# Optimization experiments

Measured on AMD Instinct MI355X. Metric: run time of the kernel, lower is better.

The kernel has to match this reference:

```python
import jax, jax.numpy as jnp
import numpy as np

B, S, D, H = 2, 2048, 1024, 16
DK = D // H

def setup_inputs() -> dict:
    key = jax.random.key(0)
    ks = jax.random.split(key, 11)
    sc = 1.0 / np.sqrt(D)
    return {
        "q": jax.random.normal(ks[0], (B, S, D), jnp.float32),
        "k": jax.random.normal(ks[1], (B, S, D), jnp.float32),
        "v": jax.random.normal(ks[2], (B, S, D), jnp.float32),
        "Wq": jax.random.normal(ks[3], (D, D), jnp.float32) * sc,
        "bq": jax.random.normal(ks[4], (D,), jnp.float32) * sc,
        "Wk": jax.random.normal(ks[5], (D, D), jnp.float32) * sc,
        "bk": jax.random.normal(ks[6], (D,), jnp.float32) * sc,
        "Wv": jax.random.normal(ks[7], (D, D), jnp.float32) * sc,
        "bv": jax.random.normal(ks[8], (D,), jnp.float32) * sc,
        "Wo": jax.random.normal(ks[9], (D, D), jnp.float32) * sc,
        "bo": jax.random.normal(ks[10], (D,), jnp.float32) * sc,
    }

def reference(q, k, v, Wq, bq, Wk, bk, Wv, bv, Wo, bo):
    b, s, d = q.shape
    # projections (torch Linear: x @ W^T + b)
    qh = (q @ Wq.T + bq).reshape(b, s, H, DK).transpose(0, 2, 1, 3)  # [B,H,S,DK]
    kh = (k @ Wk.T + bk).reshape(b, s, H, DK).transpose(0, 2, 1, 3)
    vh = (v @ Wv.T + bv).reshape(b, s, H, DK).transpose(0, 2, 1, 3)
    scores = jnp.einsum('bhqd,bhkd->bhqk', qh, kh) / jnp.sqrt(jnp.float32(DK))
    attn = jax.nn.softmax(scores, axis=-1)  # [B,H,S,S]
    out = jnp.einsum('bhqk,bhkd->bhqd', attn, vh)  # [B,H,S,DK]
    out = out.transpose(0, 2, 1, 3).reshape(b, s, d)
    return out @ Wo.T + bo
```

## Files before the change

### kernel.cpp

```cpp
#include <hip/hip_runtime.h>
#include <hip/hip_bf16.h>
#include <stdint.h>

typedef __bf16 bf16;
typedef __attribute__((ext_vector_type(8))) __bf16 bf16x8;
typedef __attribute__((ext_vector_type(4))) float f32x4;
typedef __attribute__((ext_vector_type(16))) float f32x16;
typedef __attribute__((ext_vector_type(4))) unsigned int u32x4;
typedef __attribute__((ext_vector_type(2))) unsigned int u32x2;

#define BATCH  2
#define SEQ    2048
#define DMODEL 1024
#define NH     16
#define DKH    64
#define BS     (BATCH*SEQ)
#define BSD    (BS*DMODEL)
#define DD     (DMODEL*DMODEL)

#define QSCALE 0.18033688f

__device__ __forceinline__ void gload_lds16(const bf16* g, bf16* l) {
  __builtin_amdgcn_global_load_lds((const __attribute__((address_space(1))) void*)g,
                                   (__attribute__((address_space(3))) void*)l,
                                   16, 0, 0);
}

__device__ __forceinline__ unsigned int packbf2(float a, float b) {
  union { bf16 h[2]; unsigned int u; } z;
  z.h[0] = (bf16)a; z.h[1] = (bf16)b;
  return z.u;
}

__device__ __forceinline__ float exp2_raw(float x) {
  float r;
  asm("v_exp_f32 %0, %1" : "=v"(r) : "v"(x));
  return r;
}

__device__ __forceinline__ void cvt8(const float* __restrict__ in,
                                     bf16* __restrict__ out, int i) {
  const f32x4* p = (const f32x4*)in + (size_t)i * 2;
  f32x4 a = p[0], b = p[1];
  bf16x8 o;
  o[0]=(bf16)a[0]; o[1]=(bf16)a[1]; o[2]=(bf16)a[2]; o[3]=(bf16)a[3];
  o[4]=(bf16)b[0]; o[5]=(bf16)b[1]; o[6]=(bf16)b[2]; o[7]=(bf16)b[3];
  ((bf16x8*)out)[i] = o;
}

__global__ __launch_bounds__(256) void cvt_all_kernel(
    const float* __restrict__ q, const float* __restrict__ k, const float* __restrict__ v,
    const float* __restrict__ Wq, const float* __restrict__ Wk,
    const float* __restrict__ Wv, const float* __restrict__ Wo,
    bf16* __restrict__ oq, bf16* __restrict__ ok, bf16* __restrict__ ov,
    bf16* __restrict__ oWq, bf16* __restrict__ oWk,
    bf16* __restrict__ oWv, bf16* __restrict__ oWo) {
  int i = blockIdx.x * blockDim.x + threadIdx.x;
  const int z = blockIdx.y;
  if (z == 0)      cvt8(q, oq, i);
  else if (z == 1) cvt8(k, ok, i);
  else if (z == 2) cvt8(v, ov, i);
  else {
    const int w = i >> 17;
    const int j = i & 131071;
    const float* in = (w == 0) ? Wq : (w == 1) ? Wk : (w == 2) ? Wv : Wo;
    bf16* out       = (w == 0) ? oWq : (w == 1) ? oWk : (w == 2) ? oWv : oWo;
    cvt8(in, out, j);
  }
}

template <typename OUT, int MODE, int MR>
__device__ __forceinline__ void gemm_body(const bf16* __restrict__ A,
                                          const bf16* __restrict__ W,
                                          const float* __restrict__ bias,
                                          OUT* __restrict__ C,
                                          float oscale,
                                          bf16* Als, bf16* Bls,
                                          int tx, int ty) {
  const int tid  = threadIdx.x;
  const int lane = tid & 63;
  const int wave = tid >> 6;
  const int wm = wave >> 1, wn = wave & 1;
  const int c = lane & 15, g = lane >> 4;
  const long brow = (long)ty * (MR * 32);
  const long bcol = (long)tx * 128;
  const int  N = DMODEL, K = DMODEL;
  const int  ABUF = MR * 1024;

  f32x4 acc[MR][4] = {};

  const bf16* Ag = A + (brow + wave*16 + ((lane>>2)&15)) * (long)K + (lane & 3) * 8;
  const bf16* Bg = W + (bcol + wave*16 + ((lane>>2)&15)) * (long)K + (lane & 3) * 8;

  auto stage = [&](int kt, int buf) {
    const bf16* a0 = Ag + kt * 32;
    const bf16* b0 = Bg + kt * 32;
    bf16* Ad = Als + buf * ABUF + wave * 512;
    bf16* Bd = Bls + buf * 4096 + wave * 512;
    gload_lds16(a0, Ad);
    if (MR == 4) gload_lds16(a0 + 64 * (long)K, Ad + 2048);
    gload_lds16(b0, Bd);
    gload_lds16(b0 + 64 * (long)K, Bd + 2048);
  };

  const int nk = K >> 5;
  stage(0, 0);
  int cur = 0;
  for (int kt = 0; kt < nk; ++kt) {
    __syncthreads();
    if (kt + 1 < nk) stage(kt + 1, cur ^ 1);

    bf16x8 af[MR], bfv[4];
    #pragma unroll
    for (int m = 0; m < MR; ++m)
      af[m] = *(const bf16x8*)(Als + cur * ABUF + (wm*(MR*16) + m*16 + c) * 32 + g * 8);
    #pragma unroll
    for (int n = 0; n < 4; ++n)
      bfv[n] = *(const bf16x8*)(Bls + cur * 4096 + (wn*64 + n*16 + c) * 32 + g * 8);
    __builtin_amdgcn_s_setprio(1);
    #pragma unroll
    for (int m = 0; m < MR; ++m)
      #pragma unroll
      for (int n = 0; n < 4; ++n)
        acc[m][n] = __builtin_amdgcn_mfma_f32_16x16x32_bf16(af[m], bfv[n], acc[m][n], 0, 0, 0);
    __builtin_amdgcn_s_setprio(0);
    cur ^= 1;
  }

  if (MODE == 0) {
    #pragma unroll
    for (int n = 0; n < 4; ++n) {
      const long col = bcol + wn*64 + n*16 + c;
      const float bb = bias[col];
      #pragma unroll
      for (int m = 0; m < MR; ++m) {
        #pragma unroll
        for (int r = 0; r < 4; ++r) {
          const long row = brow + wm*(MR*16) + m*16 + g*4 + r;
          C[row * (long)N + col] = (OUT)((acc[m][n][r] + bb) * oscale);
        }
      }
    }
  } else {
    const int srow = (int)(brow & (SEQ - 1));
    const int bidx = (int)(brow >> 11);
    #pragma unroll
    for (int n = 0; n < 4; ++n) {
      const int col = (int)bcol + wn*64 + n*16 + c;
      const float bb = bias[col];
      const int h = col >> 6, dk = col & 63;
      OUT* rowp = C + ((size_t)((bidx*16 + h)*64 + dk)) * SEQ + srow + wm*64;
      #pragma unroll
      for (int m = 0; m < MR; ++m) {
        u32x2 pkd;
        pkd[0] = packbf2(acc[m][n][0] + bb, acc[m][n][1] + bb);
        pkd[1] = packbf2(acc[m][n][2] + bb, acc[m][n][3] + bb);
        *(u32x2*)(rowp + m*16 + g*4) = pkd;
      }
    }
  }
}

__global__ __launch_bounds__(256) void gemm_qkv_kernel(
    const bf16* __restrict__ qb, const bf16* __restrict__ kb, const bf16* __restrict__ vb,
    const bf16* __restrict__ Wqb, const bf16* __restrict__ Wkb, const bf16* __restrict__ Wvb,
    const float* __restrict__ bq, const float* __restrict__ bk, const float* __restrict__ bv,
    bf16* __restrict__ qh, bf16* __restrict__ kh, bf16* __restrict__ vt) {
  __shared__ bf16 Als[2 * 128 * 32];
  __shared__ bf16 Bls[2 * 128 * 32];
  const int bid  = blockIdx.x + (blockIdx.y << 3) + (blockIdx.z << 8);
  const int tile = (bid & 7) * 96 + (bid >> 3);
  const int tx = tile & 7, ty = (tile >> 3) & 31, tz = tile >> 8;
  if (tz == 2) {
    gemm_body<bf16, 1, 4>(vb, Wvb, bv, vt, 1.0f, Als, Bls, tx, ty);
  } else {
    const bf16*  A  = (tz == 0) ? qb  : kb;
    const bf16*  W  = (tz == 0) ? Wqb : Wkb;
    const float* bi = (tz == 0) ? bq  : bk;
    bf16*        Cp = (tz == 0) ? qh  : kh;
    const float  os = (tz == 0) ? QSCALE : 1.0f;
    gemm_body<bf16, 0, 4>(A, W, bi, Cp, os, Als, Bls, tx, ty);
  }
}

__global__ __launch_bounds__(256) void gemm_out_kernel(
    const bf16* __restrict__ A, const bf16* __restrict__ Wob,
    const float* __restrict__ bo, float* __restrict__ C) {
  __shared__ bf16 Als[2 * 64 * 32];
  __shared__ bf16 Bls[2 * 128 * 32];
  const int bid  = blockIdx.x + (blockIdx.y << 3);
  const int tile = (bid & 7) * 64 + (bid >> 3);
  const int tx = tile & 7, ty = tile >> 3;
  gemm_body<float, 0, 2>(A, Wob, bo, C, 1.0f, Als, Bls, tx, ty);
}

__global__ __launch_bounds__(256) void attn_kernel(const bf16* __restrict__ qh,
                                                   const bf16* __restrict__ kh,
                                                   const bf16* __restrict__ vt,
                                                   bf16* __restrict__ ao) {
  __shared__ bf16 Kls[2][64 * 64];
  __shared__ bf16 Vls[2][64 * 64];

  const int tid = threadIdx.x;
  const int lane = tid & 63, wave = tid >> 6;
  const int q32 = lane & 31, hi = lane >> 5;

  const int bx  = blockIdx.x;
  const int bh  = (bx & 7) * 4 + ((bx >> 3) >> 4);
  const int qt  = (bx >> 3) & 15;
  const int b = bh >> 4, h = bh & 15;
  const long rowbase = (long)b * SEQ;
  const int q0 = qt * 128 + wave * 32;

  const bf16* qp = qh + (rowbase + q0 + q32) * DMODEL + h * 64 + hi * 8;
  bf16x8 qf[4];
  #pragma unroll
  for (int ks = 0; ks < 4; ++ks) qf[ks] = *(const bf16x8*)(qp + ks * 16);

  f32x16 accO0 = {}, accO1 = {};
  f32x16 accL  = {};

  bf16x8 ones8;
  {
    const bf16 sel = (q32 == 0) ? (bf16)1.0f : (bf16)0.0f;
    #pragma unroll
    for (int j = 0; j < 8; ++j) ones8[j] = sel;
  }

  int rd[2][4];
  #pragma unroll
  for (int hh = 0; hh < 2; ++hh) {
    const int row = q32 + 32 * hh;
    const int sw = (row & 7) << 4;
    #pragma unroll
    for (int ks = 0; ks < 4; ++ks)
      rd[hh][ks] = row * 128 + ((ks * 32 + hi * 16) ^ sw);
  }

  const int srw = tid >> 3, stc = tid & 7;
  const int soff = srw * 128 + ((stc * 16) ^ ((srw & 7) << 4));
  u32x4 kreg0, kreg1, vreg0, vreg1;

  const bf16* kp = kh + (rowbase + srw) * DMODEL + h * 64 + stc * 8;
  const bf16* vp = vt + ((size_t)bh * 64 + srw) * SEQ + stc * 8;

  auto load_tiles = [&]() {
    kreg0 = *(const u32x4*)kp;
    kreg1 = *(const u32x4*)(kp + 32 * DMODEL);
    vreg0 = *(const u32x4*)vp;
    vreg1 = *(const u32x4*)(vp + 32 * SEQ);
    kp += 64 * DMODEL;
    vp += 64;
  };
  auto write_tiles = [&](int buf) {
    char* Kb = (char*)Kls[buf];
    char* Vb = (char*)Vls[buf];
    *(u32x4*)(Kb + soff)        = kreg0;
    *(u32x4*)(Kb + soff + 4096) = kreg1;
    *(u32x4*)(Vb + soff)        = vreg0;
    *(u32x4*)(Vb + soff + 4096) = vreg1;
  };

  load_tiles();
  write_tiles(0);
  int cur = 0;
  const int NT = SEQ / 64;

  for (int t = 0; t < NT; ++t) {
    __syncthreads();
    if (t + 1 < NT) load_tiles();

    const char* Kb = (const char*)Kls[cur];
    const char* Vb = (const char*)Vls[cur];

    f32x16 s0 = {}, s1 = {};
    __builtin_amdgcn_s_setprio(1);
    #pragma unroll
    for (int ks = 0; ks < 4; ++ks) {
      bf16x8 k0 = *(const bf16x8*)(Kb + rd[0][ks]);
      s0 = __builtin_amdgcn_mfma_f32_32x32x16_bf16(k0, qf[ks], s0, 0, 0, 0);
    }
    #pragma unroll
    for (int ks = 0; ks < 4; ++ks) {
      bf16x8 k1 = *(const bf16x8*)(Kb + rd[1][ks]);
      s1 = __builtin_amdgcn_mfma_f32_32x32x16_bf16(k1, qf[ks], s1, 0, 0, 0);
    }
    __builtin_amdgcn_s_setprio(0);

    unsigned W0[4][2], W1[4][2];
    #pragma unroll
    for (int t4 = 0; t4 < 4; ++t4) {
      float a0 = exp2_raw(s0[4*t4+0]), a1 = exp2_raw(s0[4*t4+1]);
      float a2 = exp2_raw(s0[4*t4+2]), a3 = exp2_raw(s0[4*t4+3]);
      W0[t4][0] = packbf2(a0, a1); W0[t4][1] = packbf2(a2, a3);
      float b0 = exp2_raw(s1[4*t4+0]), b1 = exp2_raw(s1[4*t4+1]);
      float b2 = exp2_raw(s1[4*t4+2]), b3 = exp2_raw(s1[4*t4+3]);
      W1[t4][0] = packbf2(b0, b1); W1[t4][1] = packbf2(b2, b3);
    }

    bf16x8 Pb[4];
    #pragma unroll
    for (int ks = 0; ks < 4; ++ks) {
      const int t0 = 2 * (ks & 1);
      unsigned w0 = (ks < 2) ? W0[t0][0]     : W1[t0][0];
      unsigned w2 = (ks < 2) ? W0[t0 + 1][0] : W1[t0 + 1][0];
      unsigned w1 = (ks < 2) ? W0[t0][1]     : W1[t0][1];
      unsigned w3 = (ks < 2) ? W0[t0 + 1][1] : W1[t0 + 1][1];
      asm("v_permlane32_swap_b32 %0, %1" : "+v"(w0), "+v"(w2));
      asm("v_permlane32_swap_b32 %0, %1" : "+v"(w1), "+v"(w3));
      union { unsigned u[4]; bf16x8 v; } P;
      P.u[0] = w0; P.u[1] = w1; P.u[2] = w2; P.u[3] = w3;
      Pb[ks] = P.v;
    }

    __builtin_amdgcn_s_setprio(1);
    #pragma unroll
    for (int ks = 0; ks < 4; ++ks) {
      bf16x8 v0 = *(const bf16x8*)(Vb + rd[0][ks]);
      accO0 = __builtin_amdgcn_mfma_f32_32x32x16_bf16(v0, Pb[ks], accO0, 0, 0, 0);
    }
    #pragma unroll
    for (int ks = 0; ks < 4; ++ks) {
      bf16x8 v1 = *(const bf16x8*)(Vb + rd[1][ks]);
      accO1 = __builtin_amdgcn_mfma_f32_32x32x16_bf16(v1, Pb[ks], accO1, 0, 0, 0);
    }
    #pragma unroll
    for (int ks = 0; ks < 4; ++ks)
      accL = __builtin_amdgcn_mfma_f32_32x32x16_bf16(ones8, Pb[ks], accL, 0, 0, 0);
    __builtin_amdgcn_s_setprio(0);

    if (t + 1 < NT) write_tiles(cur ^ 1);
    cur ^= 1;
  }

  const float lall = __shfl(accL[0], q32);
  const float inv = 1.f / lall;
  bf16* dst = ao + (rowbase + q0 + q32) * DMODEL + h * 64;
  #pragma unroll
  for (int t4 = 0; t4 < 4; ++t4) {
    const int d0 = 8 * t4 + 4 * hi;
    u32x2 p0, p1;
    p0[0] = packbf2(accO0[4*t4+0] * inv, accO0[4*t4+1] * inv);
    p0[1] = packbf2(accO0[4*t4+2] * inv, accO0[4*t4+3] * inv);
    *(u32x2*)(dst + d0) = p0;
    p1[0] = packbf2(accO1[4*t4+0] * inv, accO1[4*t4+1] * inv);
    p1[1] = packbf2(accO1[4*t4+2] * inv, accO1[4*t4+3] * inv);
    *(u32x2*)(dst + d0 + 32) = p1;
  }
}

extern "C" void kernel_launch(void* const* d_in, const int* in_sizes, int n_in,
                              void* d_out, int out_size, void* d_ws, size_t ws_size,
                              hipStream_t stream) {
  const float* q  = (const float*)d_in[0];
  const float* k  = (const float*)d_in[1];
  const float* v  = (const float*)d_in[2];
  const float* Wq = (const float*)d_in[3];
  const float* bq = (const float*)d_in[4];
  const float* Wk = (const float*)d_in[5];
  const float* bk = (const float*)d_in[6];
  const float* Wv = (const float*)d_in[7];
  const float* bv = (const float*)d_in[8];
  const float* Wo = (const float*)d_in[9];
  const float* bo = (const float*)d_in[10];
  float* out = (float*)d_out;

  char* w = (char*)d_ws;
  bf16* qb  = (bf16*)w; w += (size_t)BSD * 2;
  bf16* kb  = (bf16*)w; w += (size_t)BSD * 2;
  bf16* vb  = (bf16*)w; w += (size_t)BSD * 2;
  bf16* Wqb = (bf16*)w; w += (size_t)DD * 2;
  bf16* Wkb = (bf16*)w; w += (size_t)DD * 2;
  bf16* Wvb = (bf16*)w; w += (size_t)DD * 2;
  bf16* Wob = (bf16*)w; w += (size_t)DD * 2;
  bf16* qhd = (bf16*)w; w += (size_t)BSD * 2;
  bf16* khd = (bf16*)w; w += (size_t)BSD * 2;
  bf16* vtd = (bf16*)w; w += (size_t)BSD * 2;
  bf16* aod = (bf16*)w; w += (size_t)BSD * 2;

  cvt_all_kernel<<<dim3(BSD / 8 / 256, 4), 256, 0, stream>>>(
      q, k, v, Wq, Wk, Wv, Wo, qb, kb, vb, Wqb, Wkb, Wvb, Wob);

  gemm_qkv_kernel<<<dim3(8, 32, 3), 256, 0, stream>>>(qb, kb, vb, Wqb, Wkb, Wvb,
                                                      bq, bk, bv, qhd, khd, vtd);
  attn_kernel<<<512, 256, 0, stream>>>(qhd, khd, vtd, aod);
  gemm_out_kernel<<<dim3(8, 64), 256, 0, stream>>>(aod, Wob, bo, out);
}
```

Measured before the change: 128.8 us.

## Split attention KV sequence across two wave groups per block and reduce in LDS

Doubles the attention block to 512 threads: each pair of waves shares a 32-row query slice but processes opposite halves of the key/value sequence, staging both halves' tiles into a 64KB LDS buffer. Partial output and row-sum accumulators are then combined through shared memory before normalization and store. The aim is more waves in flight per CU to hide the serial KV-loop latency, at the cost of higher LDS use, which may limit occupancy, plus an extra reduction step. The softmax has no max subtraction, so the partial sums can be added directly.

```diff
diff --git a/kernel.cpp b/kernel.cpp
--- a/kernel.cpp
+++ b/kernel.cpp
@@ -194,23 +194,25 @@
   gemm_body<float, 0, 2>(A, Wob, bo, C, 1.0f, Als, Bls, tx, ty);
 }
 
-__global__ __launch_bounds__(256) void attn_kernel(const bf16* __restrict__ qh,
+__global__ __launch_bounds__(512) void attn_kernel(const bf16* __restrict__ qh,
                                                    const bf16* __restrict__ kh,
                                                    const bf16* __restrict__ vt,
                                                    bf16* __restrict__ ao) {
-  __shared__ bf16 Kls[2][64 * 64];
-  __shared__ bf16 Vls[2][64 * 64];
+  __shared__ char smem[65536];
+  bf16* Kbase = (bf16*)smem;
+  bf16* Vbase = (bf16*)(smem + 32768);
 
   const int tid = threadIdx.x;
   const int lane = tid & 63, wave = tid >> 6;
   const int q32 = lane & 31, hi = lane >> 5;
+  const int qg = wave >> 1, half = wave & 1;
 
   const int bx  = blockIdx.x;
   const int bh  = (bx & 7) * 4 + ((bx >> 3) >> 4);
   const int qt  = (bx >> 3) & 15;
   const int b = bh >> 4, h = bh & 15;
   const long rowbase = (long)b * SEQ;
-  const int q0 = qt * 128 + wave * 32;
+  const int q0 = qt * 128 + qg * 32;
 
   const bf16* qp = qh + (rowbase + q0 + q32) * DMODEL + h * 64 + hi * 8;
   bf16x8 qf[4];
@@ -237,12 +239,14 @@
       rd[hh][ks] = row * 128 + ((ks * 32 + hi * 16) ^ sw);
   }
 
-  const int srw = tid >> 3, stc = tid & 7;
+  const int st_half = tid >> 8;
+  const int t8 = tid & 255;
+  const int srw = t8 >> 3, stc = t8 & 7;
   const int soff = srw * 128 + ((stc * 16) ^ ((srw & 7) << 4));
   u32x4 kreg0, kreg1, vreg0, vreg1;
 
-  const bf16* kp = kh + (rowbase + srw) * DMODEL + h * 64 + stc * 8;
-  const bf16* vp = vt + ((size_t)bh * 64 + srw) * SEQ + stc * 8;
+  const bf16* kp = kh + (rowbase + st_half * 1024 + srw) * DMODEL + h * 64 + stc * 8;
+  const bf16* vp = vt + ((size_t)bh * 64 + srw) * SEQ + st_half * 1024 + stc * 8;
 
   auto load_tiles = [&]() {
     kreg0 = *(const u32x4*)kp;
@@ -253,8 +257,8 @@
     vp += 64;
   };
   auto write_tiles = [&](int buf) {
-    char* Kb = (char*)Kls[buf];
-    char* Vb = (char*)Vls[buf];
+    char* Kb = (char*)(Kbase + (buf * 2 + st_half) * 4096);
+    char* Vb = (char*)(Vbase + (buf * 2 + st_half) * 4096);
     *(u32x4*)(Kb + soff)        = kreg0;
     *(u32x4*)(Kb + soff + 4096) = kreg1;
     *(u32x4*)(Vb + soff)        = vreg0;
@@ -264,14 +268,14 @@
   load_tiles();
   write_tiles(0);
   int cur = 0;
-  const int NT = SEQ / 64;
-
-  for (int t = 0; t < NT; ++t) {
+  const int NT2 = SEQ / 64 / 2;
+
+  for (int t = 0; t < NT2; ++t) {
     __syncthreads();
-    if (t + 1 < NT) load_tiles();
-
-    const char* Kb = (const char*)Kls[cur];
-    const char* Vb = (const char*)Vls[cur];
+    if (t + 1 < NT2) load_tiles();
+
+    const char* Kb = (const char*)(Kbase + (cur * 2 + half) * 4096);
+    const char* Vb = (const char*)(Vbase + (cur * 2 + half) * 4096);
 
     f32x16 s0 = {}, s1 = {};
     __builtin_amdgcn_s_setprio(1);
@@ -329,23 +333,42 @@
       accL = __builtin_amdgcn_mfma_f32_32x32x16_bf16(ones8, Pb[ks], accL, 0, 0, 0);
     __builtin_amdgcn_s_setprio(0);
 
-    if (t + 1 < NT) write_tiles(cur ^ 1);
+    if (t + 1 < NT2) write_tiles(cur ^ 1);
     cur ^= 1;
   }
 
-  const float lall = __shfl(accL[0], q32);
-  const float inv = 1.f / lall;
-  bf16* dst = ao + (rowbase + q0 + q32) * DMODEL + h * 64;
-  #pragma unroll
-  for (int t4 = 0; t4 < 4; ++t4) {
-    const int d0 = 8 * t4 + 4 * hi;
-    u32x2 p0, p1;
-    p0[0] = packbf2(accO0[4*t4+0] * inv, accO0[4*t4+1] * inv);
-    p0[1] = packbf2(accO0[4*t4+2] * inv, accO0[4*t4+3] * inv);
-    *(u32x2*)(dst + d0) = p0;
-    p1[0] = packbf2(accO1[4*t4+0] * inv, accO1[4*t4+1] * inv);
-    p1[1] = packbf2(accO1[4*t4+2] * inv, accO1[4*t4+3] * inv);
-    *(u32x2*)(dst + d0 + 32) = p1;
+  const float lpart = __shfl(accL[0], q32);
+  __syncthreads();
+  float* cb = (float*)smem + qg * 2176;
+  if (half == 1) {
+    #pragma unroll
+    for (int i = 0; i < 16; ++i) {
+      cb[lane + 64 * i]        = accO0[i];
+      cb[lane + 64 * (16 + i)] = accO1[i];
+    }
+    cb[lane + 64 * 32] = lpart;
+  }
+  __syncthreads();
+  if (half == 0) {
+    const float lall = lpart + cb[lane + 64 * 32];
+    const float inv = 1.f / lall;
+    #pragma unroll
+    for (int i = 0; i < 16; ++i) {
+      accO0[i] += cb[lane + 64 * i];
+      accO1[i] += cb[lane + 64 * (16 + i)];
+    }
+    bf16* dst = ao + (rowbase + q0 + q32) * DMODEL + h * 64;
+    #pragma unroll
+    for (int t4 = 0; t4 < 4; ++t4) {
+      const int d0 = 8 * t4 + 4 * hi;
+      u32x2 p0, p1;
+      p0[0] = packbf2(accO0[4*t4+0] * inv, accO0[4*t4+1] * inv);
+      p0[1] = packbf2(accO0[4*t4+2] * inv, accO0[4*t4+3] * inv);
+      *(u32x2*)(dst + d0) = p0;
+      p1[0] = packbf2(accO1[4*t4+0] * inv, accO1[4*t4+1] * inv);
+      p1[1] = packbf2(accO1[4*t4+2] * inv, accO1[4*t4+3] * inv);
+      *(u32x2*)(dst + d0 + 32) = p1;
+    }
   }
 }
 
@@ -383,6 +406,6 @@
 
   gemm_qkv_kernel<<<dim3(8, 32, 3), 256, 0, stream>>>(qb, kb, vb, Wqb, Wkb, Wvb,
                                                       bq, bk, bv, qhd, khd, vtd);
-  attn_kernel<<<512, 256, 0, stream>>>(qhd, khd, vtd, aod);
+  attn_kernel<<<512, 512, 0, stream>>>(qhd, khd, vtd, aod);
   gemm_out_kernel<<<dim3(8, 64), 256, 0, stream>>>(aod, Wob, bo, out);
 }
```

Measured after the change: 124.3 us. 1.04x faster.
